# Optimization experiments

Hardware: AMD Instinct MI355X
Metric: run time of the kernel (lower is better)

## Reference

```python
import jax, jax.numpy as jnp
import numpy as np

B, S, E, H = 2, 2048, 1024, 16
D = E // H  # head_dim = 64


def setup_inputs() -> dict:
    key = jax.random.key(0)
    ks = jax.random.split(key, 6)
    scale = 1.0 / np.sqrt(E)
    return {
        "x": jax.random.normal(ks[0], (B, S, E), dtype=jnp.float32),
        "Wqkv_w": jax.random.normal(ks[1], (3 * E, E), dtype=jnp.float32) * scale,
        "Wqkv_b": jax.random.normal(ks[2], (3 * E,), dtype=jnp.float32) * 0.01,
        "out_w": jax.random.normal(ks[3], (E, E), dtype=jnp.float32) * scale,
        "out_b": jax.random.normal(ks[4], (E,), dtype=jnp.float32) * 0.01,
        "distance_decay": jax.random.normal(ks[5], (1,), dtype=jnp.float32),
    }


def reference(x, Wqkv_w, Wqkv_b, out_w, out_b, distance_decay):
    b, s, e = x.shape
    # fused QKV projection: (b, s, 3e) -> three (b, h, s, d)
    qkv = x @ Wqkv_w.T + Wqkv_b
    qkv = qkv.reshape(b, s, 3, H, D).transpose(2, 0, 3, 1, 4)  # (3, b, h, s, d)
    q, k, v = qkv[0], qkv[1], qkv[2]
    # scores scaled by 1/sqrt(head_dim)
    scores = jnp.einsum("bhsd,bhtd->bhst", q, k) / jnp.sqrt(jnp.asarray(D, x.dtype))
    # multiplicative exponential distance decay: exp(-|a| * |i-j|)
    idx = jnp.arange(s, dtype=x.dtype)
    dist = jnp.abs(idx[:, None] - idx[None, :])  # (s, s)
    decay = jnp.exp(-jnp.abs(distance_decay[0]) * dist)
    scores = scores * decay  # broadcast over (b, h)
    attn = jax.nn.softmax(scores, axis=-1)
    out = jnp.einsum("bhst,bhtd->bhsd", attn, v)  # (b, h, s, d)
    out = out.transpose(0, 2, 1, 3).reshape(b, s, e)  # (b, s, e)
    return out @ out_w.T + out_b
```

## Files before the change

### kernel.cpp

```cpp
#include <hip/hip_runtime.h>
#include <hip/hip_bf16.h>

#define BN 2
#define SDIM 2048
#define EDIM 1024
#define HN 16
#define DDIM 64

typedef __attribute__((ext_vector_type(8))) short bfrag;
typedef __attribute__((ext_vector_type(4))) float ffrag;

__device__ __forceinline__ ffrag mfma16(bfrag a, bfrag b, ffrag c) {
    return __builtin_amdgcn_mfma_f32_16x16x32_bf16(a, b, c, 0, 0, 0);
}

__device__ __forceinline__ ushort f2bf(float f) {
    union { float f; unsigned u; } un;
    un.f = f;
    unsigned u = un.u;
    u += 0x7fffu + ((u >> 16) & 1u);
    return (ushort)(u >> 16);
}

__device__ __forceinline__ uint pkbf2(float a, float b) {
    __hip_bfloat162 h = __float22bfloat162_rn(make_float2(a, b));
    union { __hip_bfloat162 h; uint u; } cv;
    cv.h = h;
    return cv.u;
}

__device__ __forceinline__ void gld16(const void* g, void* l) {
    __builtin_amdgcn_global_load_lds((const __attribute__((address_space(1))) void*)g,
                                     (__attribute__((address_space(3))) void*)l,
                                     16, 0, 0);
}

__global__ __launch_bounds__(256) void to_bf16_3(const float* __restrict__ a, ushort* __restrict__ oa, int na,
                                                 const float* __restrict__ b, ushort* __restrict__ ob, int nb,
                                                 const float* __restrict__ c, ushort* __restrict__ oc, int nc) {
    int i = (blockIdx.x * 256 + threadIdx.x) * 4;
    const float* src;
    ushort* dst;
    if (i < na)                { src = a + i;            dst = oa + i; }
    else if (i < na + nb)      { src = b + (i - na);     dst = ob + (i - na); }
    else if (i < na + nb + nc) { src = c + (i - na - nb); dst = oc + (i - na - nb); }
    else return;
    float4 v = *(const float4*)src;
    uint2 u;
    u.x = pkbf2(v.x, v.y);
    u.y = pkbf2(v.z, v.w);
    *(uint2*)dst = u;
}

template <int MODE, int MI>
__global__ __launch_bounds__(256) void gemm_bt(const ushort* __restrict__ A,
                                               const ushort* __restrict__ Bt,
                                               const float* __restrict__ bias,
                                               void* __restrict__ Cout,
                                               int M, int N, int K) {
    __shared__ ushort As[MI * 32 * 64];
    __shared__ ushort Bs[128 * 64];

    const int tid  = threadIdx.x;
    const int wave = tid >> 6;
    const int lane = tid & 63;
    const int ln16 = lane & 15;
    const int quad = lane >> 4;
    const int wm = wave >> 1, wn = wave & 1;
    const int bm = blockIdx.x * (MI * 32);
    const int bn = blockIdx.y * 128;

    ffrag acc[MI][4];
#pragma unroll
    for (int mi = 0; mi < MI; ++mi)
#pragma unroll
        for (int ni = 0; ni < 4; ++ni)
            acc[mi][ni] = (ffrag){0.f, 0.f, 0.f, 0.f};

    for (int k0 = 0; k0 < K; k0 += 64) {
#pragma unroll
        for (int p = 0; p < MI; ++p) {
            int g0 = p * 256 + wave * 64;
            int g  = g0 + lane;
            int r  = g >> 3;
            int c  = ((g & 7) - r) & 7;
            gld16(A + (size_t)(bm + r) * K + k0 + c * 8, (ushort*)As + g0 * 8);
        }
#pragma unroll
        for (int p = 0; p < 4; ++p) {
            int g0 = p * 256 + wave * 64;
            int g  = g0 + lane;
            int r  = g >> 3;
            int c  = ((g & 7) - r) & 7;
            gld16(Bt + (size_t)(bn + r) * K + k0 + c * 8, (ushort*)Bs + g0 * 8);
        }
        __syncthreads();

#pragma unroll
        for (int kb = 0; kb < 2; ++kb) {
            bfrag af[MI], bf[4];
#pragma unroll
            for (int mi = 0; mi < MI; ++mi) {
                int r = wm * (MI * 16) + mi * 16 + ln16;
                af[mi] = *(const bfrag*)&As[r * 64 + ((kb * 4 + quad + r) & 7) * 8];
            }
#pragma unroll
            for (int ni = 0; ni < 4; ++ni) {
                int r = wn * 64 + ni * 16 + ln16;
                bf[ni] = *(const bfrag*)&Bs[r * 64 + ((kb * 4 + quad + r) & 7) * 8];
            }
#pragma unroll
            for (int mi = 0; mi < MI; ++mi)
#pragma unroll
                for (int ni = 0; ni < 4; ++ni)
                    acc[mi][ni] = mfma16(af[mi], bf[ni], acc[mi][ni]);
        }
        __syncthreads();
    }

#pragma unroll
    for (int mi = 0; mi < MI; ++mi) {
#pragma unroll
        for (int ni = 0; ni < 4; ++ni) {
            int col = bn + wn * 64 + ni * 16 + ln16;
            float bc = bias[col];
            int row0 = bm + wm * (MI * 16) + mi * 16 + quad * 4;
            if (MODE == 0) {
#pragma unroll
                for (int reg = 0; reg < 4; ++reg)
                    ((float*)Cout)[(size_t)(row0 + reg) * N + col] = acc[mi][ni][reg] + bc;
            } else {
                int which = col >> 10;
                int rem = col & 1023;
                int h = rem >> 6;
                int d = rem & 63;
                int b = row0 >> 11;
                int s0 = row0 & 2047;
                if (which == 2) {
                    float v0 = acc[mi][ni][0] + bc, v1 = acc[mi][ni][1] + bc;
                    float v2 = acc[mi][ni][2] + bc, v3 = acc[mi][ni][3] + bc;
                    uint2 pk;
                    pk.x = pkbf2(v0, v1);
                    pk.y = pkbf2(v2, v3);
                    size_t dst = 2ull * (BN * HN * SDIM * DDIM) +
                                 (((size_t)(b * HN + h)) * DDIM + d) * SDIM + s0;
                    *(uint2*)((ushort*)Cout + dst) = pk;
                } else {
                    float sc = (which == 0) ? 0.125f : 1.f;
#pragma unroll
                    for (int reg = 0; reg < 4; ++reg) {
                        float v = (acc[mi][ni][reg] + bc) * sc;
                        size_t dst = (size_t)which * (BN * HN * SDIM * DDIM) +
                                     (((size_t)(b * HN + h)) * SDIM + s0 + reg) * DDIM + d;
                        ((ushort*)Cout)[dst] = f2bf(v);
                    }
                }
            }
        }
    }
}

template <int UNUSED>
__global__ __launch_bounds__(512, 2) void gemm256_qkv(const ushort* __restrict__ A,
                                                      const ushort* __restrict__ Bt,
                                                      const float* __restrict__ bias,
                                                      ushort* __restrict__ Cout,
                                                      int M, int N, int K) {
    constexpr int BM = 256, BNT = 192;
    constexpr int A_USH = BM * 64;
    constexpr int B_USH = BNT * 64;
    constexpr int BUF_USH = A_USH + B_USH;
    __shared__ ushort lds[2 * BUF_USH];

    const int tid  = threadIdx.x;
    const int wave = tid >> 6;
    const int lane = tid & 63;
    const int ln16 = lane & 15;
    const int quad = lane >> 4;
    const int wm   = wave >> 2;
    const int wn   = wave & 3;
    const int bm   = blockIdx.x * BM;
    const int bn   = blockIdx.y * BNT;

    const int r0 = tid >> 3;
    const int c0 = ((tid & 7) - r0) & 7;
    const ushort* Abase = A  + (size_t)(bm + r0) * K + c0 * 8;
    const ushort* Bbase = Bt + (size_t)(bn + r0) * K + c0 * 8;
    const int ldst0 = wave * 512;

    const int Ra = wm * 128 + ln16;
    const int Rb = wn * 48 + ln16;
    int aoff[2], boff[2];
#pragma unroll
    for (int kb = 0; kb < 2; ++kb) {
        aoff[kb] = Ra * 64 + ((kb * 4 + quad + Ra) & 7) * 8;
        boff[kb] = A_USH + Rb * 64 + ((kb * 4 + quad + Rb) & 7) * 8;
    }

    ffrag acc[8][3];
#pragma unroll
    for (int mi = 0; mi < 8; ++mi)
#pragma unroll
        for (int ni = 0; ni < 3; ++ni)
            acc[mi][ni] = (ffrag){0.f, 0.f, 0.f, 0.f};

    const int nt = K >> 6;

    auto stA = [&](int buf, int t, int rnd) {
        gld16(Abase + (size_t)rnd * 64 * K + t * 64,
              &lds[buf * BUF_USH + rnd * 4096 + ldst0]);
    };
    auto stB = [&](int buf, int t, int rnd) {
        gld16(Bbase + (size_t)rnd * 64 * K + t * 64,
              &lds[buf * BUF_USH + A_USH + rnd * 4096 + ldst0]);
    };

    stA(0, 0, 0); stA(0, 0, 1); stA(0, 0, 2); stA(0, 0, 3);
    stB(0, 0, 0); stB(0, 0, 1); stB(0, 0, 2);
    stA(1, 1, 0); stA(1, 1, 2);
    stB(1, 1, 0); stB(1, 1, 1); stB(1, 1, 2);
    asm volatile("s_waitcnt vmcnt(5)" ::: "memory");
    __builtin_amdgcn_s_barrier();

    for (int t = 0; t < nt; ++t) {
        const int buf = t & 1;
        const ushort* Al = &lds[buf * BUF_USH];
        const bool h1 = (t + 1) < nt;
        const bool h2 = (t + 2) < nt;
        bfrag bfr[3][2];
#pragma unroll
        for (int p = 0; p < 4; ++p) {
            bfrag afr[2][2];
#pragma unroll
            for (int m2 = 0; m2 < 2; ++m2)
#pragma unroll
                for (int kb = 0; kb < 2; ++kb)
                    afr[m2][kb] = *(const bfrag*)(Al + aoff[kb] + (p * 2 + m2) * 1024);
            if (p == 0) {
#pragma unroll
                for (int ni = 0; ni < 3; ++ni)
#pragma unroll
                    for (int kb = 0; kb < 2; ++kb)
                        bfr[ni][kb] = *(const bfrag*)(Al + boff[kb] + ni * 1024);
            }
            if (p == 0 && h1) stA(buf ^ 1, t + 1, 1);
            if (p == 1 && h1) stA(buf ^ 1, t + 1, 3);
            if (p == 2 && h2) { stA(buf, t + 2, 0); stA(buf, t + 2, 2); stB(buf, t + 2, 0); }
            if (p == 3 && h2) { stB(buf, t + 2, 1); stB(buf, t + 2, 2); }

            __builtin_amdgcn_s_barrier();
            asm volatile("s_waitcnt lgkmcnt(0)" ::: "memory");
            __builtin_amdgcn_sched_barrier(0);
            __builtin_amdgcn_s_setprio(1);
#pragma unroll
            for (int m2 = 0; m2 < 2; ++m2)
#pragma unroll
                for (int ni = 0; ni < 3; ++ni)
#pragma unroll
                    for (int kb = 0; kb < 2; ++kb)
                        acc[p * 2 + m2][ni] = mfma16(afr[m2][kb], bfr[ni][kb], acc[p * 2 + m2][ni]);
            __builtin_amdgcn_s_setprio(0);
            if (p == 3) {
                if (h2)      { asm volatile("s_waitcnt vmcnt(5)" ::: "memory"); }
                else if (h1) { asm volatile("s_waitcnt vmcnt(0)" ::: "memory"); }
            }
            __builtin_amdgcn_s_barrier();
        }
    }

#pragma unroll
    for (int mi = 0; mi < 8; ++mi) {
#pragma unroll
        for (int ni = 0; ni < 3; ++ni) {
            int col = bn + wn * 48 + ni * 16 + ln16;
            float bc = bias[col];
            int row0 = bm + wm * 128 + mi * 16 + quad * 4;
            int which = col >> 10;
            int rem = col & 1023;
            int h = rem >> 6;
            int d = rem & 63;
            int b = row0 >> 11;
            int s0 = row0 & 2047;
            if (which == 2) {
                float v0 = acc[mi][ni][0] + bc, v1 = acc[mi][ni][1] + bc;
                float v2 = acc[mi][ni][2] + bc, v3 = acc[mi][ni][3] + bc;
                uint2 pk;
                pk.x = pkbf2(v0, v1);
                pk.y = pkbf2(v2, v3);
                size_t dst = 2ull * (BN * HN * SDIM * DDIM) +
                             (((size_t)(b * HN + h)) * DDIM + d) * SDIM + s0;
                *(uint2*)(Cout + dst) = pk;
            } else {
                float sc = (which == 0) ? 0.125f : 1.f;
#pragma unroll
                for (int reg = 0; reg < 4; ++reg) {
                    float v = (acc[mi][ni][reg] + bc) * sc;
                    size_t dst = (size_t)which * (BN * HN * SDIM * DDIM) +
                                 (((size_t)(b * HN + h)) * SDIM + s0 + reg) * DDIM + d;
                    Cout[dst] = f2bf(v);
                }
            }
        }
    }
}

__global__ __launch_bounds__(256) void vsum_tiles(const ushort* __restrict__ Vtb,
                                                  float* __restrict__ T) {
    const int bh   = blockIdx.x;
    const int tile = blockIdx.y * 4 + (threadIdx.x >> 6);
    const int d    = threadIdx.x & 63;
    const ushort* row = Vtb + ((size_t)bh * DDIM + d) * SDIM + tile * 64;
    float s = 0.f;
#pragma unroll
    for (int j = 0; j < 64; j += 8) {
        uint4 v = *(const uint4*)(row + j);
        ushort tmp[8];
        *(uint4*)tmp = v;
#pragma unroll
        for (int e = 0; e < 8; ++e) {
            union { float f; uint u; } c;
            c.u = ((uint)tmp[e]) << 16;
            s += c.f;
        }
    }
    T[((size_t)bh * 32 + tile) * 64 + d] = s;
}

__global__ __launch_bounds__(512, 4) void flash_attn(const ushort* __restrict__ Qb,
                                                     const ushort* __restrict__ Kb,
                                                     const ushort* __restrict__ Vtb,
                                                     const float* __restrict__ decay_ptr,
                                                     const float* __restrict__ T,
                                                     ushort* __restrict__ Ob) {
    __shared__ ushort KVs[2][2][4096];
    __shared__ ushort Pb[128][72];
    __shared__ float  Fv[64];

    const int tid  = threadIdx.x;
    const int wave = tid >> 6;
    const int lane = tid & 63;
    const int ln16 = lane & 15;
    const int quad = lane >> 4;

    const int bh = blockIdx.y;
    const int q0 = blockIdx.x * 128;
    const size_t head_off = (size_t)bh * SDIM * DDIM;
    const float absa = fabsf(decay_ptr[0]);
    const float LOG2E = 1.442695041f;
    const float M0L2 = -17.3123404f;
    const float E12 = 6.144212353e-6f;

    int Dstar = (absa > 1e-5f) ? (int)ceilf(16.0f / absa) : (4 * SDIM);
    int lo = q0 - 63 - Dstar; if (lo < 0) lo = 0;
    int hi = q0 + 127 + Dstar; if (hi > SDIM - 1) hi = SDIM - 1;
    const int tlo = lo >> 6;
    const int thi = hi >> 6;
    const int ntiles = thi - tlo + 1;

    if (tid < 64) {
        const float* Tp = T + (size_t)bh * 32 * 64;
        float s = 0.f;
        for (int k = 0; k < tlo; ++k)      s += Tp[k * 64 + tid];
        for (int k = thi + 1; k < 32; ++k) s += Tp[k * 64 + tid];
        Fv[tid] = s;
    }

    auto stageKV = [&](int t0, int buf) {
        int g0 = wave * 64;
        int g  = g0 + lane;
        int r  = g >> 3;
        int c  = (g - r) & 7;
        gld16(Kb  + head_off + (size_t)(t0 + r) * DDIM + c * 8,
              (ushort*)&KVs[buf][0][0] + g0 * 8);
        gld16(Vtb + head_off + (size_t)r * SDIM + t0 + c * 8,
              (ushort*)&KVs[buf][1][0] + g0 * 8);
    };

#pragma unroll
    for (int p = 0; p < 2; ++p) {
        int idx = p * 512 + tid;
        int r = idx >> 3, c = (idx & 7) * 8;
        *(uint4*)&Pb[r][c] = *(const uint4*)(Qb + head_off + (size_t)(q0 + r) * DDIM + c);
    }
    stageKV(tlo * 64, 0);
    __syncthreads();

    bfrag aq[2];
#pragma unroll
    for (int kb = 0; kb < 2; ++kb)
        aq[kb] = *(const bfrag*)&Pb[wave * 16 + ln16][kb * 32 + quad * 8];

    bfrag ones;
#pragma unroll
    for (int i = 0; i < 8; ++i) ones[i] = (short)0x3F80;

    float EcB[4], FcB[4], Epw[4], Fpw[4];
#pragma unroll
    for (int reg = 0; reg < 4; ++reg) {
        int cr = quad * 4 + reg;
        EcB[reg] = __expf(-absa * (float)(15 - cr));
        FcB[reg] = __expf(-absa * (float)cr);
    }
#pragma unroll
    for (int ni = 0; ni < 4; ++ni) {
        Epw[ni] = __expf(-absa * (float)(16 * (3 - ni)));
        Fpw[ni] = __expf(-absa * (float)(16 * ni));
    }
    const float Er = __expf(-absa * (float)ln16);
    const float Fr = __expf(-absa * (float)(15 - ln16));

    ffrag lacc = (ffrag){0.f, 0.f, 0.f, 0.f};
    ffrag o[4];
#pragma unroll
    for (int ni = 0; ni < 4; ++ni) o[ni] = (ffrag){0.f, 0.f, 0.f, 0.f};

    const int m = wave * 16 + ln16;

    for (int it = 0; it < ntiles; ++it) {
        const int t0 = (tlo + it) * 64;
        const int buf = it & 1;
        if (it + 1 < ntiles) stageKV(t0 + 64, buf ^ 1);

        const ushort* Kt = &KVs[buf][0][0];
        const ushort* Vt = &KVs[buf][1][0];

        ffrag sc[4];
#pragma unroll
        for (int ni = 0; ni < 4; ++ni) {
            ffrag a = (ffrag){0.f, 0.f, 0.f, 0.f};
            const int rk = ni * 16 + ln16;
#pragma unroll
            for (int kb = 0; kb < 2; ++kb) {
                bfrag kf = *(const bfrag*)&Kt[rk * 64 + ((kb * 4 + quad + rk) & 7) * 8];
                a = mfma16(kf, aq[kb], a);
            }
            sc[ni] = a;
        }

        const int ds = q0 + wave * 16 - t0;
        float hh = 0.f;
        if (ds >= 64)       hh = __expf(-absa * (float)(ds - 63)) * Er * LOG2E;
        else if (ds <= -16) hh = __expf(-absa * (float)(-ds - 15)) * Fr * LOG2E;

#pragma unroll
        for (int ni = 0; ni < 4; ++ni) {
            float f0, f1, f2, f3;
            if (ds >= 64) {
                float hn = hh * Epw[ni];
                f0 = hn * EcB[0]; f1 = hn * EcB[1]; f2 = hn * EcB[2]; f3 = hn * EcB[3];
            } else if (ds <= -16) {
                float hn = hh * Fpw[ni];
                f0 = hn * FcB[0]; f1 = hn * FcB[1]; f2 = hn * FcB[2]; f3 = hn * FcB[3];
            } else {
                int c0 = ni * 16 + quad * 4;
                f0 = __expf(-absa * fabsf((float)(ds + ln16 - c0)))     * LOG2E;
                f1 = __expf(-absa * fabsf((float)(ds + ln16 - c0 - 1))) * LOG2E;
                f2 = __expf(-absa * fabsf((float)(ds + ln16 - c0 - 2))) * LOG2E;
                f3 = __expf(-absa * fabsf((float)(ds + ln16 - c0 - 3))) * LOG2E;
            }
            float p0 = exp2f(fmaf(sc[ni][0], f0, M0L2));
            float p1 = exp2f(fmaf(sc[ni][1], f1, M0L2));
            float p2 = exp2f(fmaf(sc[ni][2], f2, M0L2));
            float p3 = exp2f(fmaf(sc[ni][3], f3, M0L2));
            uint2 pk;
            pk.x = pkbf2(p0, p1);
            pk.y = pkbf2(p2, p3);
            *(uint2*)&Pb[m][ni * 16 + quad * 4] = pk;
        }

        bfrag ap[2];
#pragma unroll
        for (int kb = 0; kb < 2; ++kb)
            ap[kb] = *(const bfrag*)&Pb[m][kb * 32 + quad * 8];

#pragma unroll
        for (int kb = 0; kb < 2; ++kb)
            lacc = mfma16(ones, ap[kb], lacc);
#pragma unroll
        for (int ni = 0; ni < 4; ++ni) {
            const int rv = ni * 16 + ln16;
#pragma unroll
            for (int kb = 0; kb < 2; ++kb) {
                bfrag vf = *(const bfrag*)&Vt[rv * 64 + ((kb * 4 + quad + rv) & 7) * 8];
                o[ni] = mfma16(vf, ap[kb], o[ni]);
            }
        }
        __syncthreads();
    }

    const float farl = E12 * (float)(SDIM - 64 * ntiles);
    const float inv = 1.f / (lacc[0] + farl);
    const int b = bh / HN, h = bh % HN;
    const int s = q0 + m;
    ushort* dst = Ob + ((size_t)(b * SDIM + s)) * EDIM + h * DDIM + quad * 4;
#pragma unroll
    for (int ni = 0; ni < 4; ++ni) {
        int d0 = ni * 16 + quad * 4;
        float v0 = (o[ni][0] + E12 * Fv[d0 + 0]) * inv;
        float v1 = (o[ni][1] + E12 * Fv[d0 + 1]) * inv;
        float v2 = (o[ni][2] + E12 * Fv[d0 + 2]) * inv;
        float v3 = (o[ni][3] + E12 * Fv[d0 + 3]) * inv;
        uint2 pk;
        pk.x = pkbf2(v0, v1);
        pk.y = pkbf2(v2, v3);
        *(uint2*)(dst + ni * 16) = pk;
    }
}

extern "C" void kernel_launch(void* const* d_in, const int* in_sizes, int n_in,
                              void* d_out, int out_size, void* d_ws, size_t ws_size,
                              hipStream_t stream) {
    const float* x      = (const float*)d_in[0];
    const float* Wqkv_w = (const float*)d_in[1];
    const float* Wqkv_b = (const float*)d_in[2];
    const float* out_w  = (const float*)d_in[3];
    const float* out_b  = (const float*)d_in[4];
    const float* dd     = (const float*)d_in[5];

    char* ws = (char*)d_ws;
    const size_t MB = 1024 * 1024;
    ushort* xb    = (ushort*)(ws + 0 * MB);
    ushort* wqkvb = (ushort*)(ws + 8 * MB);
    ushort* owb   = (ushort*)(ws + 14 * MB);
    ushort* qkvb  = (ushort*)(ws + 16 * MB);
    ushort* ob    = (ushort*)(ws + 40 * MB);
    float*  Tp    = (float*)(ws + 0 * MB);

    const int n_x = BN * SDIM * EDIM;
    const int n_w = 3 * EDIM * EDIM;
    const int n_o = EDIM * EDIM;
    const int HSD = BN * HN * SDIM * DDIM;

    to_bf16_3<<<(n_x + n_w + n_o) / 1024, 256, 0, stream>>>(
        x, xb, n_x, Wqkv_w, wqkvb, n_w, out_w, owb, n_o);

    gemm256_qkv<0><<<dim3(16, 16), 512, 0, stream>>>(xb, wqkvb, Wqkv_b, qkvb,
                                                     BN * SDIM, 3 * EDIM, EDIM);

    vsum_tiles<<<dim3(32, 8), 256, 0, stream>>>(qkvb + 2 * HSD, Tp);

    flash_attn<<<dim3(SDIM / 128, BN * HN), 512, 0, stream>>>(
        qkvb, qkvb + HSD, qkvb + 2 * HSD, dd, Tp, ob);

    gemm_bt<0, 2><<<dim3(64, 8), 256, 0, stream>>>(ob, owb, out_b, d_out,
                                                   BN * SDIM, EDIM, EDIM);
}
```

Before: 166.7 us.

## Replace output projection GEMM with double-buffered 128x128 tile kernel

Swaps the simple single-buffered 64x128 output-projection GEMM for a 128x128-tile, 512-thread kernel that prefetches two K-tiles ahead into double-buffered LDS, using explicit vmcnt waits, raw barriers and s_setprio around the MFMA block. This is meant to overlap global loads with MFMA work and halve the block count, cutting the per-K-step load stall of the old kernel. The old unused gemm_bt template is removed. It risks lower occupancy from the larger LDS footprint and fewer blocks (256) on a large-CU GPU.

```diff
diff --git a/kernel.cpp b/kernel.cpp
--- a/kernel.cpp
+++ b/kernel.cpp
@@ -50,114 +50,6 @@
     u.x = pkbf2(v.x, v.y);
     u.y = pkbf2(v.z, v.w);
     *(uint2*)dst = u;
-}
-
-template <int MODE, int MI>
-__global__ __launch_bounds__(256) void gemm_bt(const ushort* __restrict__ A,
-                                               const ushort* __restrict__ Bt,
-                                               const float* __restrict__ bias,
-                                               void* __restrict__ Cout,
-                                               int M, int N, int K) {
-    __shared__ ushort As[MI * 32 * 64];
-    __shared__ ushort Bs[128 * 64];
-
-    const int tid  = threadIdx.x;
-    const int wave = tid >> 6;
-    const int lane = tid & 63;
-    const int ln16 = lane & 15;
-    const int quad = lane >> 4;
-    const int wm = wave >> 1, wn = wave & 1;
-    const int bm = blockIdx.x * (MI * 32);
-    const int bn = blockIdx.y * 128;
-
-    ffrag acc[MI][4];
-#pragma unroll
-    for (int mi = 0; mi < MI; ++mi)
-#pragma unroll
-        for (int ni = 0; ni < 4; ++ni)
-            acc[mi][ni] = (ffrag){0.f, 0.f, 0.f, 0.f};
-
-    for (int k0 = 0; k0 < K; k0 += 64) {
-#pragma unroll
-        for (int p = 0; p < MI; ++p) {
-            int g0 = p * 256 + wave * 64;
-            int g  = g0 + lane;
-            int r  = g >> 3;
-            int c  = ((g & 7) - r) & 7;
-            gld16(A + (size_t)(bm + r) * K + k0 + c * 8, (ushort*)As + g0 * 8);
-        }
-#pragma unroll
-        for (int p = 0; p < 4; ++p) {
-            int g0 = p * 256 + wave * 64;
-            int g  = g0 + lane;
-            int r  = g >> 3;
-            int c  = ((g & 7) - r) & 7;
-            gld16(Bt + (size_t)(bn + r) * K + k0 + c * 8, (ushort*)Bs + g0 * 8);
-        }
-        __syncthreads();
-
-#pragma unroll
-        for (int kb = 0; kb < 2; ++kb) {
-            bfrag af[MI], bf[4];
-#pragma unroll
-            for (int mi = 0; mi < MI; ++mi) {
-                int r = wm * (MI * 16) + mi * 16 + ln16;
-                af[mi] = *(const bfrag*)&As[r * 64 + ((kb * 4 + quad + r) & 7) * 8];
-            }
-#pragma unroll
-            for (int ni = 0; ni < 4; ++ni) {
-                int r = wn * 64 + ni * 16 + ln16;
-                bf[ni] = *(const bfrag*)&Bs[r * 64 + ((kb * 4 + quad + r) & 7) * 8];
-            }
-#pragma unroll
-            for (int mi = 0; mi < MI; ++mi)
-#pragma unroll
-                for (int ni = 0; ni < 4; ++ni)
-                    acc[mi][ni] = mfma16(af[mi], bf[ni], acc[mi][ni]);
-        }
-        __syncthreads();
-    }
-
-#pragma unroll
-    for (int mi = 0; mi < MI; ++mi) {
-#pragma unroll
-        for (int ni = 0; ni < 4; ++ni) {
-            int col = bn + wn * 64 + ni * 16 + ln16;
-            float bc = bias[col];
-            int row0 = bm + wm * (MI * 16) + mi * 16 + quad * 4;
-            if (MODE == 0) {
-#pragma unroll
-                for (int reg = 0; reg < 4; ++reg)
-                    ((float*)Cout)[(size_t)(row0 + reg) * N + col] = acc[mi][ni][reg] + bc;
-            } else {
-                int which = col >> 10;
-                int rem = col & 1023;
-                int h = rem >> 6;
-                int d = rem & 63;
-                int b = row0 >> 11;
-                int s0 = row0 & 2047;
-                if (which == 2) {
-                    float v0 = acc[mi][ni][0] + bc, v1 = acc[mi][ni][1] + bc;
-                    float v2 = acc[mi][ni][2] + bc, v3 = acc[mi][ni][3] + bc;
-                    uint2 pk;
-                    pk.x = pkbf2(v0, v1);
-                    pk.y = pkbf2(v2, v3);
-                    size_t dst = 2ull * (BN * HN * SDIM * DDIM) +
-                                 (((size_t)(b * HN + h)) * DDIM + d) * SDIM + s0;
-                    *(uint2*)((ushort*)Cout + dst) = pk;
-                } else {
-                    float sc = (which == 0) ? 0.125f : 1.f;
-#pragma unroll
-                    for (int reg = 0; reg < 4; ++reg) {
-                        float v = (acc[mi][ni][reg] + bc) * sc;
-                        size_t dst = (size_t)which * (BN * HN * SDIM * DDIM) +
-                                     (((size_t)(b * HN + h)) * SDIM + s0 + reg) * DDIM + d;
-                        ((ushort*)Cout)[dst] = f2bf(v);
-                    }
-                }
-            }
-        }
-    }
 }
 
 template <int UNUSED>
@@ -300,6 +192,117 @@
                     Cout[dst] = f2bf(v);
                 }
             }
+        }
+    }
+}
+
+__global__ __launch_bounds__(512, 4) void gemm128_op(const ushort* __restrict__ A,
+                                                     const ushort* __restrict__ Bt,
+                                                     const float* __restrict__ bias,
+                                                     float* __restrict__ C,
+                                                     int M, int N, int K) {
+    constexpr int BM = 128, BNT = 128;
+    constexpr int A_USH = BM * 64;
+    constexpr int B_USH = BNT * 64;
+    constexpr int BUF_USH = A_USH + B_USH;
+    __shared__ ushort lds[2 * BUF_USH];
+
+    const int tid  = threadIdx.x;
+    const int wave = tid >> 6;
+    const int lane = tid & 63;
+    const int ln16 = lane & 15;
+    const int quad = lane >> 4;
+    const int wm   = wave >> 2;
+    const int wn   = wave & 3;
+    const int bm   = blockIdx.x * BM;
+    const int bn   = blockIdx.y * BNT;
+
+    const int r0 = tid >> 3;
+    const int c0 = ((tid & 7) - r0) & 7;
+    const ushort* Abase = A  + (size_t)(bm + r0) * K + c0 * 8;
+    const ushort* Bbase = Bt + (size_t)(bn + r0) * K + c0 * 8;
+    const int ldst0 = wave * 512;
+
+    const int Ra = wm * 64 + ln16;
+    const int Rb = wn * 32 + ln16;
+    int aoff[2], boff[2];
+#pragma unroll
+    for (int kb = 0; kb < 2; ++kb) {
+        aoff[kb] = Ra * 64 + ((kb * 4 + quad + Ra) & 7) * 8;
+        boff[kb] = A_USH + Rb * 64 + ((kb * 4 + quad + Rb) & 7) * 8;
+    }
+
+    ffrag acc[4][2];
+#pragma unroll
+    for (int mi = 0; mi < 4; ++mi)
+#pragma unroll
+        for (int ni = 0; ni < 2; ++ni)
+            acc[mi][ni] = (ffrag){0.f, 0.f, 0.f, 0.f};
+
+    const int nt = K >> 6;
+
+    auto stA = [&](int buf, int t, int rnd) {
+        gld16(Abase + (size_t)rnd * 64 * K + t * 64,
+              &lds[buf * BUF_USH + rnd * 4096 + ldst0]);
+    };
+    auto stB = [&](int buf, int t, int rnd) {
+        gld16(Bbase + (size_t)rnd * 64 * K + t * 64,
+              &lds[buf * BUF_USH + A_USH + rnd * 4096 + ldst0]);
+    };
+
+    stA(0, 0, 0); stA(0, 0, 1); stB(0, 0, 0); stB(0, 0, 1);
+    stA(1, 1, 0); stA(1, 1, 1); stB(1, 1, 0); stB(1, 1, 1);
+    asm volatile("s_waitcnt vmcnt(4)" ::: "memory");
+    __builtin_amdgcn_s_barrier();
+
+    for (int t = 0; t < nt; ++t) {
+        const int buf = t & 1;
+        const ushort* Al = &lds[buf * BUF_USH];
+        bfrag afr[4][2], bfr[2][2];
+#pragma unroll
+        for (int mi = 0; mi < 4; ++mi)
+#pragma unroll
+            for (int kb = 0; kb < 2; ++kb)
+                afr[mi][kb] = *(const bfrag*)(Al + aoff[kb] + mi * 1024);
+#pragma unroll
+        for (int ni = 0; ni < 2; ++ni)
+#pragma unroll
+            for (int kb = 0; kb < 2; ++kb)
+                bfr[ni][kb] = *(const bfrag*)(Al + boff[kb] + ni * 1024);
+        asm volatile("s_waitcnt lgkmcnt(0)" ::: "memory");
+        __builtin_amdgcn_sched_barrier(0);
+        __builtin_amdgcn_s_barrier();
+
+        if (t + 2 < nt) {
+            stA(buf, t + 2, 0); stA(buf, t + 2, 1);
+            stB(buf, t + 2, 0); stB(buf, t + 2, 1);
+        }
+
+        __builtin_amdgcn_s_setprio(1);
+#pragma unroll
+        for (int mi = 0; mi < 4; ++mi)
+#pragma unroll
+            for (int ni = 0; ni < 2; ++ni)
+#pragma unroll
+                for (int kb = 0; kb < 2; ++kb)
+                    acc[mi][ni] = mfma16(afr[mi][kb], bfr[ni][kb], acc[mi][ni]);
+        __builtin_amdgcn_s_setprio(0);
+
+        if (t + 2 < nt)      { asm volatile("s_waitcnt vmcnt(4)" ::: "memory"); }
+        else if (t + 1 < nt) { asm volatile("s_waitcnt vmcnt(0)" ::: "memory"); }
+        __builtin_amdgcn_s_barrier();
+    }
+
+#pragma unroll
+    for (int mi = 0; mi < 4; ++mi) {
+#pragma unroll
+        for (int ni = 0; ni < 2; ++ni) {
+            int col = bn + wn * 32 + ni * 16 + ln16;
+            float bc = bias[col];
+            int row0 = bm + wm * 64 + mi * 16 + quad * 4;
+#pragma unroll
+            for (int reg = 0; reg < 4; ++reg)
+                C[(size_t)(row0 + reg) * N + col] = acc[mi][ni][reg] + bc;
         }
     }
 }
@@ -542,6 +545,6 @@
     flash_attn<<<dim3(SDIM / 128, BN * HN), 512, 0, stream>>>(
         qkvb, qkvb + HSD, qkvb + 2 * HSD, dd, Tp, ob);
 
-    gemm_bt<0, 2><<<dim3(64, 8), 256, 0, stream>>>(ob, owb, out_b, d_out,
-                                                   BN * SDIM, EDIM, EDIM);
-}
+    gemm128_op<<<dim3(32, 8), 512, 0, stream>>>(ob, owb, out_b, (float*)d_out,
+                                                BN * SDIM, EDIM, EDIM);
+}
```

Result: no change. 164.2 us (-1.5%).
